# Kernel tuning notes

Measured on AMD Instinct MI355X. Metric: run time of the kernel, lower is better.

The kernel has to match this reference:

```python
import jax, jax.numpy as jnp
import numpy as np

NB_CODE = 1024
CODE_DIM = 64
N, T = 32, 8192


def setup_inputs() -> dict:
    key = jax.random.key(0)
    k1, k2 = jax.random.split(key)
    x = jax.random.normal(k1, (N, T, CODE_DIM), dtype=jnp.float32)
    codebook = jax.random.normal(k2, (NB_CODE, CODE_DIM), dtype=jnp.float32)
    return {"x": x, "codebook": codebook}


def reference(x, codebook):
    # x: [N, T, C] with C == code_dim == encdec_dim -> no projection, no transpose
    n, t, c = x.shape
    nb_code = codebook.shape[0]
    xf = x.reshape(-1, c)  # [NT, C]

    dist = (
        jnp.sum(xf * xf, axis=-1, keepdims=True)
        - 2.0 * (xf @ codebook.T)
        + jnp.sum(codebook * codebook, axis=-1)[None, :]
    )
    # eval-mode gumbel_sample(-dist) == argmax(-dist) == argmin(dist)
    code_idx = jnp.argmin(dist, axis=-1)  # [NT] int32

    # dequantize: embedding gather
    x_d = codebook[code_idx]  # [NT, C]

    # compute_perplexity (no-grad in original): one-hot scatter counts
    counts = jnp.zeros((nb_code,), dtype=xf.dtype).at[code_idx].add(1.0)
    prob = counts / jnp.sum(counts)
    perplexity = jnp.exp(-jnp.sum(prob * jnp.log(prob + 1e-7)))

    # commitment loss: mse(x, detach(x_d))
    commit_loss = jnp.mean(jnp.square(xf - jax.lax.stop_gradient(x_d)))

    # straight-through estimator
    x_out = xf + jax.lax.stop_gradient(x_d - xf)
    x_out = x_out.reshape(n, t, c)
    return x_out, commit_loss, perplexity
```

## Files before the change

### kernel.cpp

```cpp
#include <hip/hip_runtime.h>
#include <cfloat>
#include <cmath>

#define NB_CODE 1024
#define CODE_DIM 64
#define NROWS (32 * 8192)
#define NTC ((size_t)NROWS * CODE_DIM)
#define TAU 0.02f

typedef __attribute__((ext_vector_type(8))) short short8;
typedef __attribute__((ext_vector_type(4))) float f32x4;

#define W_LOSS 1024
#define W_FLAGCNT 1025
#define W_CNORM 1028
#define W_CBH 2052
#define W_CBL 34820
#define W_FLAGLIST 67588

__device__ inline unsigned short f2bf_rne(float x) {
    unsigned int u = __float_as_uint(x);
    unsigned int r = (u + 0x7FFFu + ((u >> 16) & 1u)) >> 16;
    return (unsigned short)r;
}
__device__ inline float bf2f(unsigned short h) {
    return __uint_as_float(((unsigned int)h) << 16);
}

__global__ void prep_kernel(const float* __restrict__ cb, float* __restrict__ ws) {
    int j = blockIdx.x * blockDim.x + threadIdx.x;
    if (j >= NB_CODE) return;
    float* cnorm = ws + W_CNORM;
    unsigned short* cbh = (unsigned short*)(ws + W_CBH);
    unsigned short* cbl = (unsigned short*)(ws + W_CBL);
    const float4* c4 = reinterpret_cast<const float4*>(cb + (size_t)j * CODE_DIM);
    float s = 0.f;
#pragma unroll
    for (int q = 0; q < 16; ++q) {
        float4 v = c4[q];
        float e[4] = {v.x, v.y, v.z, v.w};
#pragma unroll
        for (int u = 0; u < 4; ++u) {
            s = fmaf(e[u], e[u], s);
            float c2 = -2.f * e[u];
            unsigned short hb = f2bf_rne(c2);
            unsigned short lb = f2bf_rne(c2 - bf2f(hb));
            cbh[j * 64 + q * 4 + u] = hb;
            cbl[j * 64 + q * 4 + u] = lb;
        }
    }
    cnorm[j] = s;
}

__device__ inline void load_btile(const unsigned short* __restrict__ cbh,
                                  const unsigned short* __restrict__ cbl,
                                  const float* __restrict__ cnorm,
                                  int code, int lg,
                                  short8& bh0, short8& bh1, short8& bl0, short8& bl1,
                                  float& cn)
{
    const unsigned short* bhp = cbh + (size_t)code * 64 + 8 * lg;
    const unsigned short* blp = cbl + (size_t)code * 64 + 8 * lg;
    bh0 = *(const short8*)(bhp);
    bh1 = *(const short8*)(bhp + 32);
    bl0 = *(const short8*)(blp);
    bl1 = *(const short8*)(blp + 32);
    cn = cnorm[code];
}

__global__ __launch_bounds__(256) void vq_mfma_kernel(
    const float* __restrict__ x, const float* __restrict__ cb,
    float* __restrict__ ws, float* __restrict__ out, unsigned int flag_cap)
{
    __shared__ int lds_j[4 * 64];
    const int tid = threadIdx.x;
    const int w = tid >> 6, lane = tid & 63;
    const int lg = lane >> 4;
    const int li = lane & 15;
    const int wavebase = blockIdx.x * 256 + w * 64;

    const float* cnorm = ws + W_CNORM;
    const unsigned short* cbh = (const unsigned short*)(ws + W_CBH);
    const unsigned short* cbl = (const unsigned short*)(ws + W_CBL);
    unsigned int* counts = (unsigned int*)ws;
    float* loss_sum = ws + W_LOSS;
    unsigned int* flagcnt = (unsigned int*)ws + W_FLAGCNT;
    unsigned int* flaglist = (unsigned int*)ws + W_FLAGLIST;

    short8 ah[4][2], al[4][2];
    float x2sum = 0.f;
#pragma unroll
    for (int rt = 0; rt < 4; ++rt) {
        const float* xr = x + (size_t)(wavebase + rt * 16 + li) * CODE_DIM;
#pragma unroll
        for (int f = 0; f < 2; ++f) {
            const float4* p = reinterpret_cast<const float4*>(xr + 32 * f + 8 * lg);
            float4 v0 = p[0], v1 = p[1];
            float e[8] = {v0.x, v0.y, v0.z, v0.w, v1.x, v1.y, v1.z, v1.w};
            short8 h8, l8;
#pragma unroll
            for (int i = 0; i < 8; ++i) {
                float xe = e[i];
                x2sum = fmaf(xe, xe, x2sum);
                unsigned short hb = f2bf_rne(xe);
                unsigned short lb = f2bf_rne(xe - bf2f(hb));
                h8[i] = (short)hb;
                l8[i] = (short)lb;
            }
            ah[rt][f] = h8;
            al[rt][f] = l8;
        }
    }

    float best[4][4], second[4][4];
    int bestj[4][4];
#pragma unroll
    for (int rt = 0; rt < 4; ++rt)
#pragma unroll
        for (int r = 0; r < 4; ++r) {
            best[rt][r] = FLT_MAX; second[rt][r] = FLT_MAX; bestj[rt][r] = 0;
        }

    short8 bh0, bh1, bl0, bl1; float cn;
    load_btile(cbh, cbl, cnorm, li, lg, bh0, bh1, bl0, bl1, cn);
    for (int t = 0; t < 64; ++t) {
        short8 nh0, nh1, nl0, nl1; float ncn;
        load_btile(cbh, cbl, cnorm, ((t + 1) & 63) * 16 + li, lg, nh0, nh1, nl0, nl1, ncn);
        const int code = t * 16 + li;
        f32x4 cinit = {cn, cn, cn, cn};
#pragma unroll
        for (int rt = 0; rt < 4; ++rt) {
            f32x4 acc = __builtin_amdgcn_mfma_f32_16x16x32_bf16(ah[rt][0], bh0, cinit, 0, 0, 0);
            acc = __builtin_amdgcn_mfma_f32_16x16x32_bf16(ah[rt][1], bh1, acc, 0, 0, 0);
            acc = __builtin_amdgcn_mfma_f32_16x16x32_bf16(al[rt][0], bh0, acc, 0, 0, 0);
            acc = __builtin_amdgcn_mfma_f32_16x16x32_bf16(al[rt][1], bh1, acc, 0, 0, 0);
            acc = __builtin_amdgcn_mfma_f32_16x16x32_bf16(ah[rt][0], bl0, acc, 0, 0, 0);
            acc = __builtin_amdgcn_mfma_f32_16x16x32_bf16(ah[rt][1], bl1, acc, 0, 0, 0);
#pragma unroll
            for (int r = 0; r < 4; ++r) {
                float d = acc[r];
                float mx = fmaxf(best[rt][r], d);
                second[rt][r] = fminf(second[rt][r], mx);
                bool take = d < best[rt][r];
                best[rt][r] = take ? d : best[rt][r];
                bestj[rt][r] = take ? code : bestj[rt][r];
            }
        }
        bh0 = nh0; bh1 = nh1; bl0 = nl0; bl1 = nl1; cn = ncn;
    }

#pragma unroll
    for (int rt = 0; rt < 4; ++rt)
#pragma unroll
        for (int r = 0; r < 4; ++r) {
            float b = best[rt][r], s = second[rt][r];
            int j = bestj[rt][r];
#pragma unroll
            for (int m = 1; m <= 8; m <<= 1) {
                float ob = __shfl_xor(b, m, 64);
                float os = __shfl_xor(s, m, 64);
                int   oj = __shfl_xor(j, m, 64);
                float s2 = fminf(fminf(s, os), fmaxf(b, ob));
                bool take = (ob < b) || (ob == b && oj < j);
                b = take ? ob : b;
                j = take ? oj : j;
                s = s2;
            }
            best[rt][r] = b; second[rt][r] = s; bestj[rt][r] = j;
        }

    float lsum = x2sum;
    if (li == 0) {
#pragma unroll
        for (int rt = 0; rt < 4; ++rt)
#pragma unroll
            for (int r = 0; r < 4; ++r) {
                int rowin = rt * 16 + lg * 4 + r;
                int j = bestj[rt][r];
                lds_j[w * 64 + rowin] = j;
                atomicAdd(&counts[j], 1u);
                lsum += best[rt][r];
                if (second[rt][r] - best[rt][r] <= TAU) {
                    unsigned pos = atomicAdd(flagcnt, 1u);
                    if (pos < flag_cap)
                        flaglist[pos] = ((unsigned)(wavebase + rowin) << 10) | (unsigned)j;
                }
            }
    }
#pragma unroll
    for (int m = 32; m >= 1; m >>= 1) lsum += __shfl_down(lsum, m, 64);
    if (lane == 0) atomicAdd(loss_sum, lsum);

    __syncthreads();

    for (int it = 0; it < 16; ++it) {
        int rowin = it * 4 + lg;
        int j = lds_j[w * 64 + rowin];
        float4 v = *reinterpret_cast<const float4*>(cb + (size_t)j * CODE_DIM + li * 4);
        *reinterpret_cast<float4*>(out + (size_t)(wavebase + rowin) * CODE_DIM + li * 4) = v;
    }
}

__global__ __launch_bounds__(256) void fixup_kernel(
    const float* __restrict__ x, const float* __restrict__ cb,
    float* __restrict__ ws, float* __restrict__ out, unsigned int flag_cap)
{
    unsigned nf = *((unsigned*)ws + W_FLAGCNT);
    if (nf > flag_cap) nf = flag_cap;
    const float* cnorm = ws + W_CNORM;
    unsigned* flaglist = (unsigned*)ws + W_FLAGLIST;
    unsigned* counts = (unsigned*)ws;

    const int lane = threadIdx.x & 63;
    const unsigned wave_id = (blockIdx.x * blockDim.x + threadIdx.x) >> 6;
    const unsigned nwaves = (gridDim.x * blockDim.x) >> 6;

    for (unsigned idx = wave_id; idx < nf; idx += nwaves) {
        unsigned e = flaglist[idx];
        int row = (int)(e >> 10);
        int oldj = (int)(e & 1023u);

        float xr[CODE_DIM];
        const float4* x4 = reinterpret_cast<const float4*>(x + (size_t)row * CODE_DIM);
#pragma unroll
        for (int q = 0; q < 16; ++q) {
            float4 v = x4[q];
            xr[4 * q + 0] = v.x; xr[4 * q + 1] = v.y;
            xr[4 * q + 2] = v.z; xr[4 * q + 3] = v.w;
        }

        float bestv = FLT_MAX; int bj = 0x7fffffff;
        for (int t = 0; t < 16; ++t) {
            int j = lane * 16 + t;
            const float* c = cb + (size_t)j * CODE_DIM;
            float d0 = 0.f, d1 = 0.f, d2 = 0.f, d3 = 0.f;
#pragma unroll
            for (int k = 0; k < CODE_DIM; k += 4) {
                d0 = fmaf(xr[k + 0], c[k + 0], d0);
                d1 = fmaf(xr[k + 1], c[k + 1], d1);
                d2 = fmaf(xr[k + 2], c[k + 2], d2);
                d3 = fmaf(xr[k + 3], c[k + 3], d3);
            }
            float dist = fmaf(-2.f, (d0 + d1) + (d2 + d3), cnorm[j]);
            if (dist < bestv) { bestv = dist; bj = j; }
        }
#pragma unroll
        for (int m = 1; m <= 32; m <<= 1) {
            float ob = __shfl_xor(bestv, m, 64);
            int   oj = __shfl_xor(bj, m, 64);
            bool take = (ob < bestv) || (ob == bestv && oj < bj);
            bestv = take ? ob : bestv;
            bj = take ? oj : bestv == bestv ? (take ? oj : bj) : bj;
            if (take) bj = oj;
        }

        if (bj != oldj) {
            if (lane < 16) {
                *reinterpret_cast<float4*>(out + (size_t)row * CODE_DIM + lane * 4) =
                    *reinterpret_cast<const float4*>(cb + (size_t)bj * CODE_DIM + lane * 4);
            }
            if (lane == 0) {
                atomicAdd(&counts[bj], 1u);
                atomicAdd(&counts[oldj], (unsigned)-1);
            }
        }
    }
}

__global__ void finalize_kernel(const unsigned int* __restrict__ counts,
                                const float* __restrict__ loss_sum,
                                float* __restrict__ out)
{
    __shared__ float red[NB_CODE];
    int t = threadIdx.x;
    float p = (float)counts[t] / (float)NROWS;
    red[t] = p * logf(p + 1e-7f);
    __syncthreads();
    for (int s = NB_CODE / 2; s > 0; s >>= 1) {
        if (t < s) red[t] += red[t + s];
        __syncthreads();
    }
    if (t == 0) {
        out[NTC + 0] = *loss_sum / (float)NTC;
        out[NTC + 1] = expf(-red[0]);
    }
}

extern "C" void kernel_launch(void* const* d_in, const int* in_sizes, int n_in,
                              void* d_out, int out_size, void* d_ws, size_t ws_size,
                              hipStream_t stream) {
    const float* x  = (const float*)d_in[0];
    const float* cb = (const float*)d_in[1];
    float* out = (float*)d_out;
    float* ws = (float*)d_ws;

    unsigned flag_cap = 0;
    size_t words = ws_size / 4;
    if (words > (size_t)W_FLAGLIST) flag_cap = (unsigned)(words - W_FLAGLIST);
    if (flag_cap > NROWS) flag_cap = NROWS;

    hipMemsetAsync(d_ws, 0, 1028 * sizeof(float), stream);

    prep_kernel<<<NB_CODE / 256, 256, 0, stream>>>(cb, ws);
    vq_mfma_kernel<<<NROWS / 256, 256, 0, stream>>>(x, cb, ws, out, flag_cap);
    fixup_kernel<<<256, 256, 0, stream>>>(x, cb, ws, out, flag_cap);
    finalize_kernel<<<1, NB_CODE, 0, stream>>>((unsigned int*)ws, ws + W_LOSS, out);
}
```

Measured before the change: 339.1 us.

## Pre-swizzle codebook into MFMA fragment layout and double-buffer B tiles

```diff
diff --git a/kernel.cpp b/kernel.cpp
--- a/kernel.cpp
+++ b/kernel.cpp
@@ -14,8 +14,7 @@
 #define W_LOSS 1024
 #define W_FLAGCNT 1025
 #define W_CNORM 1028
-#define W_CBH 2052
-#define W_CBL 34820
+#define W_CBP 2052
 #define W_FLAGLIST 67588
 
 __device__ inline unsigned short f2bf_rne(float x) {
@@ -31,8 +30,10 @@
     int j = blockIdx.x * blockDim.x + threadIdx.x;
     if (j >= NB_CODE) return;
     float* cnorm = ws + W_CNORM;
-    unsigned short* cbh = (unsigned short*)(ws + W_CBH);
-    unsigned short* cbl = (unsigned short*)(ws + W_CBL);
+    unsigned short* cbp = (unsigned short*)(ws + W_CBP);
+    const int t = j >> 4, li = j & 15;
+
+    float c2v[CODE_DIM];
     const float4* c4 = reinterpret_cast<const float4*>(cb + (size_t)j * CODE_DIM);
     float s = 0.f;
 #pragma unroll
@@ -42,30 +43,44 @@
 #pragma unroll
         for (int u = 0; u < 4; ++u) {
             s = fmaf(e[u], e[u], s);
-            float c2 = -2.f * e[u];
-            unsigned short hb = f2bf_rne(c2);
-            unsigned short lb = f2bf_rne(c2 - bf2f(hb));
-            cbh[j * 64 + q * 4 + u] = hb;
-            cbl[j * 64 + q * 4 + u] = lb;
+            c2v[q * 4 + u] = -2.f * e[u];
         }
     }
     cnorm[j] = s;
-}
-
-__device__ inline void load_btile(const unsigned short* __restrict__ cbh,
-                                  const unsigned short* __restrict__ cbl,
-                                  const float* __restrict__ cnorm,
-                                  int code, int lg,
-                                  short8& bh0, short8& bh1, short8& bl0, short8& bl1,
-                                  float& cn)
+
+#pragma unroll
+    for (int f = 0; f < 2; ++f) {
+#pragma unroll
+        for (int lg = 0; lg < 4; ++lg) {
+            short8 h8, l8;
+#pragma unroll
+            for (int i = 0; i < 8; ++i) {
+                float c2 = c2v[32 * f + 8 * lg + i];
+                unsigned short hb = f2bf_rne(c2);
+                unsigned short lb = f2bf_rne(c2 - bf2f(hb));
+                h8[i] = (short)hb;
+                l8[i] = (short)lb;
+            }
+            size_t ehi = ((size_t)(t * 4 + f) * 64 + lg * 16 + li);
+            size_t elo = ((size_t)(t * 4 + 2 + f) * 64 + lg * 16 + li);
+            *reinterpret_cast<short8*>(cbp + ehi * 8) = h8;
+            *reinterpret_cast<short8*>(cbp + elo * 8) = l8;
+        }
+    }
+}
+
+struct BTile { short8 b0, b1, b2, b3; float cn; };
+
+__device__ inline void load_tile(const unsigned short* __restrict__ cbp,
+                                 const float* __restrict__ cnorm,
+                                 int t, int lane, int li, BTile& T)
 {
-    const unsigned short* bhp = cbh + (size_t)code * 64 + 8 * lg;
-    const unsigned short* blp = cbl + (size_t)code * 64 + 8 * lg;
-    bh0 = *(const short8*)(bhp);
-    bh1 = *(const short8*)(bhp + 32);
-    bl0 = *(const short8*)(blp);
-    bl1 = *(const short8*)(blp + 32);
-    cn = cnorm[code];
+    const unsigned short* base = cbp + ((size_t)t * 4 * 64 + lane) * 8;
+    T.b0 = *reinterpret_cast<const short8*>(base);
+    T.b1 = *reinterpret_cast<const short8*>(base + 64 * 8);
+    T.b2 = *reinterpret_cast<const short8*>(base + 128 * 8);
+    T.b3 = *reinterpret_cast<const short8*>(base + 192 * 8);
+    T.cn = cnorm[t * 16 + li];
 }
 
 __global__ __launch_bounds__(256) void vq_mfma_kernel(
@@ -80,8 +95,7 @@
     const int wavebase = blockIdx.x * 256 + w * 64;
 
     const float* cnorm = ws + W_CNORM;
-    const unsigned short* cbh = (const unsigned short*)(ws + W_CBH);
-    const unsigned short* cbl = (const unsigned short*)(ws + W_CBL);
+    const unsigned short* cbp = (const unsigned short*)(ws + W_CBP);
     unsigned int* counts = (unsigned int*)ws;
     float* loss_sum = ws + W_LOSS;
     unsigned int* flagcnt = (unsigned int*)ws + W_FLAGCNT;
@@ -121,33 +135,41 @@
             best[rt][r] = FLT_MAX; second[rt][r] = FLT_MAX; bestj[rt][r] = 0;
         }
 
-    short8 bh0, bh1, bl0, bl1; float cn;
-    load_btile(cbh, cbl, cnorm, li, lg, bh0, bh1, bl0, bl1, cn);
-    for (int t = 0; t < 64; ++t) {
-        short8 nh0, nh1, nl0, nl1; float ncn;
-        load_btile(cbh, cbl, cnorm, ((t + 1) & 63) * 16 + li, lg, nh0, nh1, nl0, nl1, ncn);
-        const int code = t * 16 + li;
-        f32x4 cinit = {cn, cn, cn, cn};
-#pragma unroll
-        for (int rt = 0; rt < 4; ++rt) {
-            f32x4 acc = __builtin_amdgcn_mfma_f32_16x16x32_bf16(ah[rt][0], bh0, cinit, 0, 0, 0);
-            acc = __builtin_amdgcn_mfma_f32_16x16x32_bf16(ah[rt][1], bh1, acc, 0, 0, 0);
-            acc = __builtin_amdgcn_mfma_f32_16x16x32_bf16(al[rt][0], bh0, acc, 0, 0, 0);
-            acc = __builtin_amdgcn_mfma_f32_16x16x32_bf16(al[rt][1], bh1, acc, 0, 0, 0);
-            acc = __builtin_amdgcn_mfma_f32_16x16x32_bf16(ah[rt][0], bl0, acc, 0, 0, 0);
-            acc = __builtin_amdgcn_mfma_f32_16x16x32_bf16(ah[rt][1], bl1, acc, 0, 0, 0);
-#pragma unroll
-            for (int r = 0; r < 4; ++r) {
-                float d = acc[r];
-                float mx = fmaxf(best[rt][r], d);
-                second[rt][r] = fminf(second[rt][r], mx);
-                bool take = d < best[rt][r];
-                best[rt][r] = take ? d : best[rt][r];
-                bestj[rt][r] = take ? code : bestj[rt][r];
-            }
-        }
-        bh0 = nh0; bh1 = nh1; bl0 = nl0; bl1 = nl1; cn = ncn;
-    }
+    BTile A, B;
+    load_tile(cbp, cnorm, 0, lane, li, A);
+    load_tile(cbp, cnorm, 1, lane, li, B);
+
+#define COMPUTE_TILE(T, tt)                                                          \
+    {                                                                                \
+        const int code = (tt) * 16 + li;                                             \
+        f32x4 cinit = {T.cn, T.cn, T.cn, T.cn};                                      \
+        _Pragma("unroll")                                                            \
+        for (int rt = 0; rt < 4; ++rt) {                                             \
+            f32x4 acc = __builtin_amdgcn_mfma_f32_16x16x32_bf16(ah[rt][0], T.b0, cinit, 0, 0, 0); \
+            acc = __builtin_amdgcn_mfma_f32_16x16x32_bf16(ah[rt][1], T.b1, acc, 0, 0, 0); \
+            acc = __builtin_amdgcn_mfma_f32_16x16x32_bf16(al[rt][0], T.b0, acc, 0, 0, 0); \
+            acc = __builtin_amdgcn_mfma_f32_16x16x32_bf16(al[rt][1], T.b1, acc, 0, 0, 0); \
+            acc = __builtin_amdgcn_mfma_f32_16x16x32_bf16(ah[rt][0], T.b2, acc, 0, 0, 0); \
+            acc = __builtin_amdgcn_mfma_f32_16x16x32_bf16(ah[rt][1], T.b3, acc, 0, 0, 0); \
+            _Pragma("unroll")                                                        \
+            for (int r = 0; r < 4; ++r) {                                            \
+                float d = acc[r];                                                    \
+                float mx = fmaxf(best[rt][r], d);                                    \
+                second[rt][r] = fminf(second[rt][r], mx);                            \
+                bool take = d < best[rt][r];                                         \
+                best[rt][r] = take ? d : best[rt][r];                                \
+                bestj[rt][r] = take ? code : bestj[rt][r];                           \
+            }                                                                        \
+        }                                                                            \
+    }
+
+    for (int t = 0; t < 64; t += 2) {
+        COMPUTE_TILE(A, t);
+        load_tile(cbp, cnorm, (t + 2) & 63, lane, li, A);
+        COMPUTE_TILE(B, t + 1);
+        load_tile(cbp, cnorm, (t + 3) & 63, lane, li, B);
+    }
+#undef COMPUTE_TILE
 
 #pragma unroll
     for (int rt = 0; rt < 4; ++rt)
@@ -249,9 +271,7 @@
             float ob = __shfl_xor(bestv, m, 64);
             int   oj = __shfl_xor(bj, m, 64);
             bool take = (ob < bestv) || (ob == bestv && oj < bj);
-            bestv = take ? ob : bestv;
-            bj = take ? oj : bestv == bestv ? (take ? oj : bj) : bj;
-            if (take) bj = oj;
+            if (take) { bestv = ob; bj = oj; }
         }
 
         if (bj != oldj) {
```

Measured after the change: 291.5 us. 1.16x faster.

## Stage bf16 codebook in LDS, drop low-part MFMAs, pack code index into distance bits

Applied to the files above, without the earlier changes.

```diff
diff --git a/kernel.cpp b/kernel.cpp
--- a/kernel.cpp
+++ b/kernel.cpp
@@ -6,7 +6,7 @@
 #define CODE_DIM 64
 #define NROWS (32 * 8192)
 #define NTC ((size_t)NROWS * CODE_DIM)
-#define TAU 0.02f
+#define TAU 0.15f
 
 typedef __attribute__((ext_vector_type(8))) short short8;
 typedef __attribute__((ext_vector_type(4))) float f32x4;
@@ -15,8 +15,7 @@
 #define W_FLAGCNT 1025
 #define W_CNORM 1028
 #define W_CBH 2052
-#define W_CBL 34820
-#define W_FLAGLIST 67588
+#define W_FLAGLIST 34820
 
 __device__ inline unsigned short f2bf_rne(float x) {
     unsigned int u = __float_as_uint(x);
@@ -25,6 +24,9 @@
 }
 __device__ inline float bf2f(unsigned short h) {
     return __uint_as_float(((unsigned int)h) << 16);
+}
+__device__ inline float unmask6(float v) {
+    return __uint_as_float(__float_as_uint(v) & 0xFFFFFFC0u);
 }
 
 __global__ void prep_kernel(const float* __restrict__ cb, float* __restrict__ ws) {
@@ -32,7 +34,9 @@
     if (j >= NB_CODE) return;
     float* cnorm = ws + W_CNORM;
     unsigned short* cbh = (unsigned short*)(ws + W_CBH);
-    unsigned short* cbl = (unsigned short*)(ws + W_CBL);
+    const int t = j >> 4, li = j & 15;
+
+    float c2v[CODE_DIM];
     const float4* c4 = reinterpret_cast<const float4*>(cb + (size_t)j * CODE_DIM);
     float s = 0.f;
 #pragma unroll
@@ -42,46 +46,41 @@
 #pragma unroll
         for (int u = 0; u < 4; ++u) {
             s = fmaf(e[u], e[u], s);
-            float c2 = -2.f * e[u];
-            unsigned short hb = f2bf_rne(c2);
-            unsigned short lb = f2bf_rne(c2 - bf2f(hb));
-            cbh[j * 64 + q * 4 + u] = hb;
-            cbl[j * 64 + q * 4 + u] = lb;
+            c2v[q * 4 + u] = -2.f * e[u];
         }
     }
     cnorm[j] = s;
-}
-
-__device__ inline void load_btile(const unsigned short* __restrict__ cbh,
-                                  const unsigned short* __restrict__ cbl,
-                                  const float* __restrict__ cnorm,
-                                  int code, int lg,
-                                  short8& bh0, short8& bh1, short8& bl0, short8& bl1,
-                                  float& cn)
-{
-    const unsigned short* bhp = cbh + (size_t)code * 64 + 8 * lg;
-    const unsigned short* blp = cbl + (size_t)code * 64 + 8 * lg;
-    bh0 = *(const short8*)(bhp);
-    bh1 = *(const short8*)(bhp + 32);
-    bl0 = *(const short8*)(blp);
-    bl1 = *(const short8*)(blp + 32);
-    cn = cnorm[code];
-}
-
-__global__ __launch_bounds__(256) void vq_mfma_kernel(
+
+#pragma unroll
+    for (int f = 0; f < 2; ++f) {
+#pragma unroll
+        for (int lg = 0; lg < 4; ++lg) {
+            short8 h8;
+#pragma unroll
+            for (int i = 0; i < 8; ++i)
+                h8[i] = (short)f2bf_rne(c2v[32 * f + 8 * lg + i]);
+            size_t e = ((size_t)(t * 2 + f) * 64 + lg * 16 + li);
+            *reinterpret_cast<short8*>(cbh + e * 8) = h8;
+        }
+    }
+}
+
+__global__ __launch_bounds__(512, 4) void vq_mfma_kernel(
     const float* __restrict__ x, const float* __restrict__ cb,
     float* __restrict__ ws, float* __restrict__ out, unsigned int flag_cap)
 {
-    __shared__ int lds_j[4 * 64];
+    __shared__ short8 sB[4096];
+    __shared__ float scn[NB_CODE];
+    __shared__ int lds_j[8 * 64];
+
     const int tid = threadIdx.x;
     const int w = tid >> 6, lane = tid & 63;
     const int lg = lane >> 4;
     const int li = lane & 15;
-    const int wavebase = blockIdx.x * 256 + w * 64;
-
-    const float* cnorm = ws + W_CNORM;
-    const unsigned short* cbh = (const unsigned short*)(ws + W_CBH);
-    const unsigned short* cbl = (const unsigned short*)(ws + W_CBL);
+    const int wavebase = blockIdx.x * 512 + w * 64;
+
+    const float* cnorm_g = ws + W_CNORM;
+    const short8* cbh_v = (const short8*)(ws + W_CBH);
     unsigned int* counts = (unsigned int*)ws;
     float* loss_sum = ws + W_LOSS;
     unsigned int* flagcnt = (unsigned int*)ws + W_FLAGCNT;
@@ -103,9 +102,8 @@
                 float xe = e[i];
                 x2sum = fmaf(xe, xe, x2sum);
                 unsigned short hb = f2bf_rne(xe);
-                unsigned short lb = f2bf_rne(xe - bf2f(hb));
                 h8[i] = (short)hb;
-                l8[i] = (short)lb;
+                l8[i] = (short)f2bf_rne(xe - bf2f(hb));
             }
             ah[rt][f] = h8;
             al[rt][f] = l8;
@@ -113,60 +111,58 @@
     }
 
     float best[4][4], second[4][4];
-    int bestj[4][4];
 #pragma unroll
     for (int rt = 0; rt < 4; ++rt)
 #pragma unroll
-        for (int r = 0; r < 4; ++r) {
-            best[rt][r] = FLT_MAX; second[rt][r] = FLT_MAX; bestj[rt][r] = 0;
-        }
-
-    short8 bh0, bh1, bl0, bl1; float cn;
-    load_btile(cbh, cbl, cnorm, li, lg, bh0, bh1, bl0, bl1, cn);
-    for (int t = 0; t < 64; ++t) {
-        short8 nh0, nh1, nl0, nl1; float ncn;
-        load_btile(cbh, cbl, cnorm, ((t + 1) & 63) * 16 + li, lg, nh0, nh1, nl0, nl1, ncn);
-        const int code = t * 16 + li;
-        f32x4 cinit = {cn, cn, cn, cn};
-#pragma unroll
-        for (int rt = 0; rt < 4; ++rt) {
-            f32x4 acc = __builtin_amdgcn_mfma_f32_16x16x32_bf16(ah[rt][0], bh0, cinit, 0, 0, 0);
-            acc = __builtin_amdgcn_mfma_f32_16x16x32_bf16(ah[rt][1], bh1, acc, 0, 0, 0);
-            acc = __builtin_amdgcn_mfma_f32_16x16x32_bf16(al[rt][0], bh0, acc, 0, 0, 0);
-            acc = __builtin_amdgcn_mfma_f32_16x16x32_bf16(al[rt][1], bh1, acc, 0, 0, 0);
-            acc = __builtin_amdgcn_mfma_f32_16x16x32_bf16(ah[rt][0], bl0, acc, 0, 0, 0);
-            acc = __builtin_amdgcn_mfma_f32_16x16x32_bf16(ah[rt][1], bl1, acc, 0, 0, 0);
-#pragma unroll
-            for (int r = 0; r < 4; ++r) {
-                float d = acc[r];
-                float mx = fmaxf(best[rt][r], d);
-                second[rt][r] = fminf(second[rt][r], mx);
-                bool take = d < best[rt][r];
-                best[rt][r] = take ? d : best[rt][r];
-                bestj[rt][r] = take ? code : bestj[rt][r];
-            }
-        }
-        bh0 = nh0; bh1 = nh1; bl0 = nl0; bl1 = nl1; cn = ncn;
-    }
-
+        for (int r = 0; r < 4; ++r) { best[rt][r] = FLT_MAX; second[rt][r] = FLT_MAX; }
+
+    for (int h = 0; h < 2; ++h) {
+        __syncthreads();
+        for (int i = tid; i < 4096; i += 512) sB[i] = cbh_v[h * 4096 + i];
+        if (h == 0)
+            for (int i = tid; i < NB_CODE; i += 512) scn[i] = cnorm_g[i];
+        __syncthreads();
+
+        for (int tl = 0; tl < 32; ++tl) {
+            const int T = h * 32 + tl;
+            short8 b0 = sB[(tl * 2 + 0) * 64 + lane];
+            short8 b1 = sB[(tl * 2 + 1) * 64 + lane];
+            float cn = scn[T * 16 + li];
+            f32x4 ci = {cn, cn, cn, cn};
+#pragma unroll
+            for (int rt = 0; rt < 4; ++rt) {
+                f32x4 acc = __builtin_amdgcn_mfma_f32_16x16x32_bf16(ah[rt][0], b0, ci, 0, 0, 0);
+                acc = __builtin_amdgcn_mfma_f32_16x16x32_bf16(ah[rt][1], b1, acc, 0, 0, 0);
+                acc = __builtin_amdgcn_mfma_f32_16x16x32_bf16(al[rt][0], b0, acc, 0, 0, 0);
+                acc = __builtin_amdgcn_mfma_f32_16x16x32_bf16(al[rt][1], b1, acc, 0, 0, 0);
+#pragma unroll
+                for (int r = 0; r < 4; ++r) {
+                    float p = __uint_as_float((__float_as_uint(acc[r]) & 0xFFFFFFC0u) | (unsigned)T);
+                    float mx = fmaxf(best[rt][r], p);
+                    second[rt][r] = fminf(second[rt][r], mx);
+                    best[rt][r] = fminf(best[rt][r], p);
+                }
+            }
+        }
+    }
+
+    int codef[4][4];
 #pragma unroll
     for (int rt = 0; rt < 4; ++rt)
 #pragma unroll
         for (int r = 0; r < 4; ++r) {
             float b = best[rt][r], s = second[rt][r];
-            int j = bestj[rt][r];
+            int code = ((int)(__float_as_uint(b) & 63u) << 4) | li;
 #pragma unroll
             for (int m = 1; m <= 8; m <<= 1) {
                 float ob = __shfl_xor(b, m, 64);
                 float os = __shfl_xor(s, m, 64);
-                int   oj = __shfl_xor(j, m, 64);
-                float s2 = fminf(fminf(s, os), fmaxf(b, ob));
-                bool take = (ob < b) || (ob == b && oj < j);
-                b = take ? ob : b;
-                j = take ? oj : j;
-                s = s2;
-            }
-            best[rt][r] = b; second[rt][r] = s; bestj[rt][r] = j;
+                int   oc = __shfl_xor(code, m, 64);
+                s = fminf(fminf(s, os), fmaxf(b, ob));
+                bool take = (ob < b) || (ob == b && oc < code);
+                if (take) { b = ob; code = oc; }
+            }
+            best[rt][r] = b; second[rt][r] = s; codef[rt][r] = code;
         }
 
     float lsum = x2sum;
@@ -176,11 +172,12 @@
 #pragma unroll
             for (int r = 0; r < 4; ++r) {
                 int rowin = rt * 16 + lg * 4 + r;
-                int j = bestj[rt][r];
+                int j = codef[rt][r];
                 lds_j[w * 64 + rowin] = j;
                 atomicAdd(&counts[j], 1u);
-                lsum += best[rt][r];
-                if (second[rt][r] - best[rt][r] <= TAU) {
+                float bd = unmask6(best[rt][r]);
+                lsum += bd;
+                if (unmask6(second[rt][r]) - bd <= TAU) {
                     unsigned pos = atomicAdd(flagcnt, 1u);
                     if (pos < flag_cap)
                         flaglist[pos] = ((unsigned)(wavebase + rowin) << 10) | (unsigned)j;
@@ -249,9 +246,7 @@
             float ob = __shfl_xor(bestv, m, 64);
             int   oj = __shfl_xor(bj, m, 64);
             bool take = (ob < bestv) || (ob == bestv && oj < bj);
-            bestv = take ? ob : bestv;
-            bj = take ? oj : bestv == bestv ? (take ? oj : bj) : bj;
-            if (take) bj = oj;
+            if (take) { bestv = ob; bj = oj; }
         }
 
         if (bj != oldj) {
@@ -302,7 +297,7 @@
     hipMemsetAsync(d_ws, 0, 1028 * sizeof(float), stream);
 
     prep_kernel<<<NB_CODE / 256, 256, 0, stream>>>(cb, ws);
-    vq_mfma_kernel<<<NROWS / 256, 256, 0, stream>>>(x, cb, ws, out, flag_cap);
-    fixup_kernel<<<256, 256, 0, stream>>>(x, cb, ws, out, flag_cap);
+    vq_mfma_kernel<<<NROWS / 512, 512, 0, stream>>>(x, cb, ws, out, flag_cap);
+    fixup_kernel<<<768, 256, 0, stream>>>(x, cb, ws, out, flag_cap);
     finalize_kernel<<<1, NB_CODE, 0, stream>>>((unsigned int*)ws, ws + W_LOSS, out);
 }
```

Result: slower. 508.6 us (+50.0%).
